# Kernel tuning notes

Hardware: AMD Instinct MI355X
Metric: run time of the kernel (lower is better)

## Reference

```python
import jax, jax.numpy as jnp
import numpy as np

D_MODEL, D_K, D_V, N_HEADS = 1024, 64, 64, 16
BATCH, N_CTX = 2, 2048


def half_causal_allowed(n):
    # rows [0, n/2): attend to cols [0, n/2) only (dense block)
    # rows [n/2, n): standard causal (col <= row)
    i = jnp.arange(n)[:, None]
    j = jnp.arange(n)[None, :]
    top = (i < n // 2) & (j < n // 2)
    bot = (i >= n // 2) & (j <= i)
    return top | bot  # [n, n] bool


def setup_inputs() -> dict:
    key = jax.random.key(0)
    ks = jax.random.split(key, 8)
    s_in = 1.0 / np.sqrt(D_MODEL)
    s_out = 1.0 / np.sqrt(D_V * N_HEADS)
    return {
        "x": jax.random.normal(ks[0], (BATCH, N_CTX, D_MODEL), jnp.float32),
        # Linear weights stored [in, out] (transpose of torch layout)
        "Wq": jax.random.uniform(ks[1], (D_MODEL, D_K * N_HEADS), jnp.float32, -s_in, s_in),
        "bq": jax.random.uniform(ks[2], (D_K * N_HEADS,), jnp.float32, -s_in, s_in),
        "Wk": jax.random.uniform(ks[3], (D_MODEL, D_K * N_HEADS), jnp.float32, -s_in, s_in),
        "bk": jax.random.uniform(ks[4], (D_K * N_HEADS,), jnp.float32, -s_in, s_in),
        "Wv": jax.random.uniform(ks[5], (D_MODEL, D_V * N_HEADS), jnp.float32, -s_in, s_in),
        "bv": jax.random.uniform(ks[6], (D_V * N_HEADS,), jnp.float32, -s_in, s_in),
        "Wo": jax.random.uniform(ks[7], (D_V * N_HEADS, D_MODEL), jnp.float32, -s_out, s_out),
    }


def reference(x, Wq, bq, Wk, bk, Wv, bv, Wo):
    b, n, _ = x.shape
    h, dk, dv = N_HEADS, D_K, D_V
    # projections -> [b, h, n, d]
    q = (x @ Wq + bq).reshape(b, n, h, dk).transpose(0, 2, 1, 3)
    k = (x @ Wk + bk).reshape(b, n, h, dk).transpose(0, 2, 1, 3)
    v = (x @ Wv + bv).reshape(b, n, h, dv).transpose(0, 2, 1, 3)
    scores = jnp.einsum("bhqd,bhkd->bhqk", q / jnp.sqrt(jnp.float32(dk)), k)
    allowed = half_causal_allowed(n)  # [n, n]
    scores = jnp.where(allowed, scores, -jnp.inf)
    attn = jax.nn.softmax(scores, axis=-1)  # dropout p=0 -> identity
    out = jnp.einsum("bhqk,bhkd->bhqd", attn, v)
    out = out.transpose(0, 2, 1, 3).reshape(b, n, h * dv)
    return out @ Wo  # final Linear has no bias
```

## Files before the change

### kernel.cpp

```cpp
#include <hip/hip_runtime.h>
#include <hip/hip_bf16.h>

#define NH 16
#define DH 64
#define DM 1024
#define NC 2048
#define MROWS 4096
#define KVT 64

#define SCALE_Q 0.180336880f

typedef __attribute__((ext_vector_type(8))) short short8;
typedef __attribute__((ext_vector_type(4))) float f32x4;
typedef __attribute__((ext_vector_type(16))) float f32x16;
typedef __attribute__((ext_vector_type(4))) unsigned int uint4e;

__device__ __forceinline__ unsigned pkbf16(float a, float b) {
    unsigned r;
    asm("v_cvt_pk_bf16_f32 %0, %1, %2" : "=v"(r) : "v"(a), "v"(b));
    return r;
}
__device__ __forceinline__ unsigned short f2bf(float x) {
    return (unsigned short)(pkbf16(x, x) & 0xffffu);
}
__device__ __forceinline__ float exp2v(float x) {
    float r;
    asm("v_exp_f32 %0, %1" : "=v"(r) : "v"(x));
    return r;
}
__device__ __forceinline__ f32x16 fzero16() {
    f32x16 r;
    #pragma unroll
    for (int i = 0; i < 16; ++i) r[i] = 0.f;
    return r;
}
__device__ __forceinline__ short8 mk8(unsigned w0, unsigned w1, unsigned w2, unsigned w3) {
    uint4e u = {w0, w1, w2, w3};
    return __builtin_bit_cast(short8, u);
}
__device__ __forceinline__ void gload16(const unsigned short* g, unsigned short* l) {
    __builtin_amdgcn_global_load_lds(
        (const __attribute__((address_space(1))) void*)g,
        (__attribute__((address_space(3))) void*)l, 16, 0, 0);
}

__global__ __launch_bounds__(256) void cvt_x(const float* __restrict__ in,
                                             unsigned short* __restrict__ out, int n8)
{
    int i = blockIdx.x * 256 + threadIdx.x;
    if (i >= n8) return;
    const float4 a = ((const float4*)in)[i * 2];
    const float4 b = ((const float4*)in)[i * 2 + 1];
    uint4e u = {pkbf16(a.x, a.y), pkbf16(a.z, a.w), pkbf16(b.x, b.y), pkbf16(b.z, b.w)};
    ((uint4e*)out)[i] = u;
}

__global__ __launch_bounds__(256) void cvt_w4(const float* __restrict__ W0,
                                              const float* __restrict__ W1,
                                              const float* __restrict__ W2,
                                              const float* __restrict__ W3,
                                              unsigned short* __restrict__ Wt4)
{
    __shared__ unsigned short T[64][72];
    const int z = blockIdx.z;
    const float* W = (z == 0) ? W0 : (z == 1) ? W1 : (z == 2) ? W2 : W3;
    unsigned short* Wt = Wt4 + (size_t)z * DM * DM;
    const int t = threadIdx.x;
    const int r = t >> 2, s = t & 3;
    const int bi = blockIdx.y;
    const int bj = blockIdx.x;
    const float* src = W + (size_t)(bi * 64 + r) * DM + bj * 64 + s * 16;
    float4 f0 = ((const float4*)src)[0];
    float4 f1 = ((const float4*)src)[1];
    float4 f2 = ((const float4*)src)[2];
    float4 f3 = ((const float4*)src)[3];
    uint2 u;
    u.x = pkbf16(f0.x, f0.y); u.y = pkbf16(f0.z, f0.w); *(uint2*)&T[r][s * 16]      = u;
    u.x = pkbf16(f1.x, f1.y); u.y = pkbf16(f1.z, f1.w); *(uint2*)&T[r][s * 16 + 4]  = u;
    u.x = pkbf16(f2.x, f2.y); u.y = pkbf16(f2.z, f2.w); *(uint2*)&T[r][s * 16 + 8]  = u;
    u.x = pkbf16(f3.x, f3.y); u.y = pkbf16(f3.z, f3.w); *(uint2*)&T[r][s * 16 + 12] = u;
    __syncthreads();
    unsigned short vals[16];
    #pragma unroll
    for (int j = 0; j < 16; ++j) vals[j] = T[s * 16 + j][r];
    unsigned short* dst = Wt + (size_t)(bj * 64 + r) * DM + bi * 64 + s * 16;
    *(short8*)(dst)     = *(short8*)&vals[0];
    *(short8*)(dst + 8) = *(short8*)&vals[8];
}

__global__ __launch_bounds__(256) void gemm_qkv(const unsigned short* __restrict__ A,
                                                const unsigned short* __restrict__ Bt,
                                                const float* __restrict__ bq,
                                                const float* __restrict__ bk,
                                                const float* __restrict__ bv,
                                                unsigned short* __restrict__ Out)
{
    __shared__ unsigned short As[128 * 32];
    __shared__ unsigned short Bs[128 * 32];
    const int t  = threadIdx.x;
    const int w  = t >> 6, l = t & 63;
    const int wr = w >> 1, wc = w & 1;
    const int m0 = blockIdx.y << 7;
    const int n0 = blockIdx.x << 7;

    f32x4 acc[4][4] = {};
    const int nkt = DM >> 5;
    for (int kt = 0; kt < nkt; ++kt) {
        #pragma unroll
        for (int j = 0; j < 2; ++j) {
            const int c0 = j * 256 + w * 64;
            const int cc = c0 + l;
            const int row = cc >> 2, qq = cc & 3;
            gload16(A  + (size_t)(m0 + row) * DM + kt * 32 + qq * 8, &As[c0 * 8]);
            gload16(Bt + (size_t)(n0 + row) * DM + kt * 32 + qq * 8, &Bs[c0 * 8]);
        }
        __syncthreads();
        short8 af[4], bf_[4];
        #pragma unroll
        for (int mi = 0; mi < 4; ++mi)
            af[mi] = *(short8*)&As[(wr * 64 + mi * 16 + (l & 15)) * 32 + (l >> 4) * 8];
        #pragma unroll
        for (int ni = 0; ni < 4; ++ni)
            bf_[ni] = *(short8*)&Bs[(wc * 64 + ni * 16 + (l & 15)) * 32 + (l >> 4) * 8];
        #pragma unroll
        for (int mi = 0; mi < 4; ++mi)
            #pragma unroll
            for (int ni = 0; ni < 4; ++ni)
                acc[mi][ni] = __builtin_amdgcn_mfma_f32_16x16x32_bf16(
                                  af[mi], bf_[ni], acc[mi][ni], 0, 0, 0);
        __syncthreads();
    }

    const int seg = n0 >> 10;
    const float* bias = (seg == 0) ? bq : (seg == 1) ? bk : bv;
    const float scale = (seg == 0) ? SCALE_Q : 1.0f;
    const int ncol0 = (n0 & 1023) + wc * 64;
    float bvv[4];
    #pragma unroll
    for (int ni = 0; ni < 4; ++ni)
        bvv[ni] = bias[ncol0 + ni * 16 + (l & 15)];

    if (seg == 2) {
        unsigned short* vt = Out + 2 * (size_t)MROWS * DM;
        #pragma unroll
        for (int mi = 0; mi < 4; ++mi)
            #pragma unroll
            for (int ni = 0; ni < 4; ++ni) {
                const int gcol = ncol0 + ni * 16 + (l & 15);
                const int h_ = gcol >> 6, d_ = gcol & 63;
                #pragma unroll
                for (int r = 0; r < 4; ++r) {
                    const int grow = m0 + wr * 64 + mi * 16 + (l >> 4) * 4 + r;
                    const int b_ = grow >> 11, n_ = grow & 2047;
                    vt[(((size_t)b_ * 16 + h_) * 64 + d_) * NC + n_] =
                        f2bf(acc[mi][ni][r] + bvv[ni]);
                }
            }
    } else {
        unsigned short* C = Out + (size_t)seg * MROWS * DM;
        #pragma unroll
        for (int mi = 0; mi < 4; ++mi)
            #pragma unroll
            for (int ni = 0; ni < 4; ++ni) {
                const int gcol = ncol0 + ni * 16 + (l & 15);
                #pragma unroll
                for (int r = 0; r < 4; ++r) {
                    const int grow = m0 + wr * 64 + mi * 16 + (l >> 4) * 4 + r;
                    C[(size_t)grow * DM + gcol] = f2bf((acc[mi][ni][r] + bvv[ni]) * scale);
                }
            }
    }
}

__global__ __launch_bounds__(256) void gemm_wo(const unsigned short* __restrict__ A,
                                               const unsigned short* __restrict__ Bt,
                                               float* __restrict__ C)
{
    __shared__ unsigned short As[64 * 32];
    __shared__ unsigned short Bs[128 * 32];
    const int t = threadIdx.x, w = t >> 6, l = t & 63;
    const int wr = w >> 1, wc = w & 1;
    const int m0 = blockIdx.y << 6;
    const int n0 = blockIdx.x << 7;

    f32x4 acc[2][4] = {};
    const int nkt = DM >> 5;
    for (int kt = 0; kt < nkt; ++kt) {
        {
            const int c0 = w * 64;
            const int cc = c0 + l;
            const int row = cc >> 2, qq = cc & 3;
            gload16(A + (size_t)(m0 + row) * DM + kt * 32 + qq * 8, &As[c0 * 8]);
        }
        #pragma unroll
        for (int j = 0; j < 2; ++j) {
            const int c0 = j * 256 + w * 64;
            const int cc = c0 + l;
            const int row = cc >> 2, qq = cc & 3;
            gload16(Bt + (size_t)(n0 + row) * DM + kt * 32 + qq * 8, &Bs[c0 * 8]);
        }
        __syncthreads();
        short8 af[2], bf_[4];
        #pragma unroll
        for (int mi = 0; mi < 2; ++mi)
            af[mi] = *(short8*)&As[(wr * 32 + mi * 16 + (l & 15)) * 32 + (l >> 4) * 8];
        #pragma unroll
        for (int ni = 0; ni < 4; ++ni)
            bf_[ni] = *(short8*)&Bs[(wc * 64 + ni * 16 + (l & 15)) * 32 + (l >> 4) * 8];
        #pragma unroll
        for (int mi = 0; mi < 2; ++mi)
            #pragma unroll
            for (int ni = 0; ni < 4; ++ni)
                acc[mi][ni] = __builtin_amdgcn_mfma_f32_16x16x32_bf16(
                                  af[mi], bf_[ni], acc[mi][ni], 0, 0, 0);
        __syncthreads();
    }
    #pragma unroll
    for (int mi = 0; mi < 2; ++mi)
        #pragma unroll
        for (int ni = 0; ni < 4; ++ni) {
            const int gcol = n0 + wc * 64 + ni * 16 + (l & 15);
            #pragma unroll
            for (int r = 0; r < 4; ++r) {
                const int grow = m0 + wr * 32 + mi * 16 + (l >> 4) * 4 + r;
                C[(size_t)grow * DM + gcol] = acc[mi][ni][r];
            }
        }
}

__global__ __launch_bounds__(128, 2) void attn_lds(const unsigned short* __restrict__ Qg,
                                                   const unsigned short* __restrict__ Kg,
                                                   const unsigned short* __restrict__ Vtg,
                                                   unsigned short* __restrict__ Og)
{
    __shared__ unsigned short KS[2][4096];
    __shared__ unsigned short VS[2][4096];
    const int t   = threadIdx.x;
    const int w   = t >> 6;
    const int l   = t & 63;
    const int l31 = l & 31;
    const int hi  = l >> 5;

    const int f   = blockIdx.x;
    const int xcd = f & 7;
    const int pos = f >> 3;
    const int bh  = xcd * 4 + (pos >> 5);
    int qt = pos & 31;
    if ((pos >> 5) & 1) qt = 31 - qt;
    const int b = bh >> 4;
    const int h = bh & 15;

    const int qb = qt << 6;
    const int wq = qb + w * 32;
    const size_t rb0 = (size_t)b * NC;
    const int hd = h * DH;

    const unsigned short* qp = Qg + (rb0 + wq + l31) * DM + hd + hi * 8;
    short8 fq[4];
    #pragma unroll
    for (int c = 0; c < 4; ++c)
        fq[c] = *(const short8*)(qp + c * 16);

    f32x16 o0 = fzero16(), o1 = fzero16();
    float mrun = -1e30f, lrun = 0.f;
    const bool bottom = (qb >= NC / 2);
    const int nkv = bottom ? (qt + 1) : 16;

    const unsigned short* Vbase = Vtg + (size_t)bh * 64 * NC;

    auto stage = [&](int it, int buf) {
        const int kb = it * KVT;
        #pragma unroll
        for (int j = 0; j < 4; ++j) {
            const int jj  = w * 4 + j;
            const int p   = jj * 64 + l;
            const int row = p >> 3;
            const int slot = (p & 7) ^ (row & 7);
            gload16(Kg + (size_t)(rb0 + kb + row) * DM + hd + slot * 8,
                    &KS[buf][jj * 512]);
            gload16(Vbase + (size_t)row * NC + kb + slot * 8,
                    &VS[buf][jj * 512]);
        }
    };

    stage(0, 0);
    __syncthreads();

    for (int it = 0; it < nkv; ++it) {
        const int kb = it * KVT;
        const int cur = it & 1;
        if (it + 1 < nkv) stage(it + 1, cur ^ 1);

        const unsigned short* Kb = &KS[cur][0];
        short8 kf[2][4];
        #pragma unroll
        for (int half = 0; half < 2; ++half) {
            const int row = half * 32 + l31;
            const int rx  = row & 7;
            #pragma unroll
            for (int c = 0; c < 4; ++c) {
                const int slot = (c * 2 + hi) ^ rx;
                kf[half][c] = *(const short8*)(Kb + row * 64 + slot * 8);
            }
        }
        f32x16 s0 = fzero16(), s1 = fzero16();
        __builtin_amdgcn_s_setprio(1);
        #pragma unroll
        for (int c = 0; c < 4; ++c) {
            s0 = __builtin_amdgcn_mfma_f32_32x32x16_bf16(kf[0][c], fq[c], s0, 0, 0, 0);
            s1 = __builtin_amdgcn_mfma_f32_32x32x16_bf16(kf[1][c], fq[c], s1, 0, 0, 0);
        }
        __builtin_amdgcn_s_setprio(0);
        if (bottom && (kb + KVT - 1 > wq)) {
            const int qg = wq + l31;
            #pragma unroll
            for (int r = 0; r < 16; ++r) {
                const int kk = (r & 3) + 8 * (r >> 2) + 4 * hi;
                if (kb + kk > qg)      s0[r] = -1e30f;
                if (kb + 32 + kk > qg) s1[r] = -1e30f;
            }
        }
        float tm[16];
        #pragma unroll
        for (int r = 0; r < 16; ++r) tm[r] = fmaxf(s0[r], s1[r]);
        #pragma unroll
        for (int st = 8; st > 0; st >>= 1)
            #pragma unroll
            for (int r = 0; r < 8; ++r)
                if (r < st) tm[r] = fmaxf(tm[r], tm[r + st]);
        float pm = fmaxf(tm[0], __shfl_xor(tm[0], 32));
        if (!__all(pm - mrun <= 8.f)) {
            const float mnew = fmaxf(mrun, pm);
            const float corr = exp2v(mrun - mnew);
            mrun = mnew;
            lrun *= corr;
            #pragma unroll
            for (int i = 0; i < 16; ++i) { o0[i] *= corr; o1[i] *= corr; }
        }
        float rs = 0.f;
        #pragma unroll
        for (int r = 0; r < 16; ++r) { s0[r] = exp2v(s0[r] - mrun); rs += s0[r]; }
        #pragma unroll
        for (int r = 0; r < 16; ++r) { s1[r] = exp2v(s1[r] - mrun); rs += s1[r]; }
        rs += __shfl_xor(rs, 32);
        lrun += rs;
        const unsigned short* Vb = &VS[cur][0];
        __builtin_amdgcn_s_setprio(1);
        #pragma unroll
        for (int kc = 0; kc < 4; ++kc) {
            const f32x16 src = (kc < 2) ? s0 : s1;
            const int rbase = (kc & 1) * 8;
            unsigned A01 = pkbf16(src[rbase + 0], src[rbase + 1]);
            unsigned A23 = pkbf16(src[rbase + 2], src[rbase + 3]);
            unsigned A45 = pkbf16(src[rbase + 4], src[rbase + 5]);
            unsigned A67 = pkbf16(src[rbase + 6], src[rbase + 7]);
            unsigned s01 = (unsigned)__shfl_xor((int)A01, 32);
            unsigned s23 = (unsigned)__shfl_xor((int)A23, 32);
            unsigned s45 = (unsigned)__shfl_xor((int)A45, 32);
            unsigned s67 = (unsigned)__shfl_xor((int)A67, 32);
            short8 fp = hi ? mk8(s45, s67, A45, A67)
                           : mk8(A01, A23, s01, s23);
            const int slot = (kc * 2 + hi);
            const int r0_ = l31, r1_ = 32 + l31;
            short8 v0 = *(const short8*)(Vb + r0_ * 64 + (slot ^ (r0_ & 7)) * 8);
            short8 v1 = *(const short8*)(Vb + r1_ * 64 + (slot ^ (r1_ & 7)) * 8);
            o0 = __builtin_amdgcn_mfma_f32_32x32x16_bf16(v0, fp, o0, 0, 0, 0);
            o1 = __builtin_amdgcn_mfma_f32_32x32x16_bf16(v1, fp, o1, 0, 0, 0);
        }
        __builtin_amdgcn_s_setprio(0);

        __syncthreads();
    }

    const float inv = 1.f / lrun;
    unsigned short* obuf = (unsigned short*)&KS[0][0];
    {
        unsigned short* reg = obuf + (size_t)(w * 32 + l31) * 72;
        #pragma unroll
        for (int r = 0; r < 16; ++r) {
            const int dd = (r & 3) + 8 * (r >> 2) + 4 * hi;
            reg[dd]      = f2bf(o0[r] * inv);
            reg[dd + 32] = f2bf(o1[r] * inv);
        }
    }
    __syncthreads();
    {
        const int row = t >> 1, seg = t & 1;
        const unsigned short* src = obuf + (size_t)row * 72 + seg * 32;
        unsigned short* dst = Og + (rb0 + qb + row) * DM + hd + seg * 32;
        #pragma unroll
        for (int i = 0; i < 4; ++i)
            *(short8*)(dst + i * 8) = *(const short8*)(src + i * 8);
    }
}

extern "C" void kernel_launch(void* const* d_in, const int* in_sizes, int n_in,
                              void* d_out, int out_size, void* d_ws, size_t ws_size,
                              hipStream_t stream)
{
    const float* x  = (const float*)d_in[0];
    const float* Wq = (const float*)d_in[1];
    const float* bq = (const float*)d_in[2];
    const float* Wk = (const float*)d_in[3];
    const float* bk = (const float*)d_in[4];
    const float* Wv = (const float*)d_in[5];
    const float* bv = (const float*)d_in[6];
    const float* Wo = (const float*)d_in[7];
    float* out = (float*)d_out;

    char* ws = (char*)d_ws;
    const size_t szA = (size_t)MROWS * DM * 2;
    const size_t szW = (size_t)DM * DM * 2;
    unsigned short* xb  = (unsigned short*)(ws);
    unsigned short* wqT = (unsigned short*)(ws + szA);
    unsigned short* woT = (unsigned short*)(ws + szA + 3 * szW);
    unsigned short* qb_ = (unsigned short*)(ws + szA + 4 * szW);
    unsigned short* kb_ = (unsigned short*)(ws + 2 * szA + 4 * szW);
    unsigned short* vt_ = (unsigned short*)(ws + 3 * szA + 4 * szW);
    unsigned short* ab_ = (unsigned short*)(ws + 4 * szA + 4 * szW);

    cvt_x<<<dim3(MROWS * DM / 8 / 256), 256, 0, stream>>>(x, xb, MROWS * DM / 8);
    cvt_w4<<<dim3(16, 16, 4), 256, 0, stream>>>(Wq, Wk, Wv, Wo, wqT);

    gemm_qkv<<<dim3(24, 32), 256, 0, stream>>>(xb, wqT, bq, bk, bv, qb_);
    attn_lds<<<dim3(1024), 128, 0, stream>>>(qb_, kb_, vt_, ab_);
    gemm_wo<<<dim3(8, 64), 256, 0, stream>>>(ab_, woT, out);
}
```

Before: 124.0 us.

## Convert attention to single-wave blocks with 32-row KV tiles and vmcnt waits

The attention kernel now uses 64-thread single-wave blocks, each owning 32 query rows, and launches twice as many blocks. KV tiles shrink to 32 keys, which halves LDS per block. Because only one wave runs per block, __syncthreads are dropped in favour of explicit s_waitcnt vmcnt waits on the double-buffered global-to-LDS loads. The aim is finer-grained load balance over the causal half and less barrier overhead, at the cost of more loop iterations, less K/V reuse across waves, and more global traffic for K/V.

```diff
diff --git a/kernel.cpp b/kernel.cpp
--- a/kernel.cpp
+++ b/kernel.cpp
@@ -6,7 +6,7 @@
 #define DM 1024
 #define NC 2048
 #define MROWS 4096
-#define KVT 64
+#define KVT 32
 
 #define SCALE_Q 0.180336880f
 
@@ -228,34 +228,31 @@
         }
 }
 
-__global__ __launch_bounds__(128, 2) void attn_lds(const unsigned short* __restrict__ Qg,
+__global__ __launch_bounds__(64, 2) void attn_wave(const unsigned short* __restrict__ Qg,
                                                    const unsigned short* __restrict__ Kg,
                                                    const unsigned short* __restrict__ Vtg,
                                                    unsigned short* __restrict__ Og)
 {
-    __shared__ unsigned short KS[2][4096];
-    __shared__ unsigned short VS[2][4096];
-    const int t   = threadIdx.x;
-    const int w   = t >> 6;
-    const int l   = t & 63;
+    __shared__ unsigned short KS[2][2048];
+    __shared__ unsigned short VS[2][2048];
+    const int l   = threadIdx.x;
     const int l31 = l & 31;
     const int hi  = l >> 5;
 
     const int f   = blockIdx.x;
     const int xcd = f & 7;
     const int pos = f >> 3;
-    const int bh  = xcd * 4 + (pos >> 5);
-    int qt = pos & 31;
-    if ((pos >> 5) & 1) qt = 31 - qt;
+    const int bh  = xcd * 4 + (pos >> 6);
+    int qt = pos & 63;
+    if ((pos >> 6) & 1) qt = 63 - qt;
     const int b = bh >> 4;
     const int h = bh & 15;
 
-    const int qb = qt << 6;
-    const int wq = qb + w * 32;
+    const int qb = qt << 5;
     const size_t rb0 = (size_t)b * NC;
     const int hd = h * DH;
 
-    const unsigned short* qp = Qg + (rb0 + wq + l31) * DM + hd + hi * 8;
+    const unsigned short* qp = Qg + (rb0 + qb + l31) * DM + hd + hi * 8;
     short8 fq[4];
     #pragma unroll
     for (int c = 0; c < 4; ++c)
@@ -264,7 +261,7 @@
     f32x16 o0 = fzero16(), o1 = fzero16();
     float mrun = -1e30f, lrun = 0.f;
     const bool bottom = (qb >= NC / 2);
-    const int nkv = bottom ? (qt + 1) : 16;
+    const int nkv = bottom ? (qt + 1) : 32;
 
     const unsigned short* Vbase = Vtg + (size_t)bh * 64 * NC;
 
@@ -272,61 +269,55 @@
         const int kb = it * KVT;
         #pragma unroll
         for (int j = 0; j < 4; ++j) {
-            const int jj  = w * 4 + j;
-            const int p   = jj * 64 + l;
-            const int row = p >> 3;
-            const int slot = (p & 7) ^ (row & 7);
-            gload16(Kg + (size_t)(rb0 + kb + row) * DM + hd + slot * 8,
-                    &KS[buf][jj * 512]);
-            gload16(Vbase + (size_t)row * NC + kb + slot * 8,
-                    &VS[buf][jj * 512]);
+            const int pk  = j * 64 + l;
+            const int krow = pk >> 3, kslot = (pk & 7) ^ (krow & 7);
+            gload16(Kg + (size_t)(rb0 + kb + krow) * DM + hd + kslot * 8,
+                    &KS[buf][j * 512]);
+            const int vrow = pk >> 2, vslot = (pk & 3) ^ (vrow & 3);
+            gload16(Vbase + (size_t)vrow * NC + kb + vslot * 8,
+                    &VS[buf][j * 512]);
         }
     };
 
     stage(0, 0);
-    __syncthreads();
 
     for (int it = 0; it < nkv; ++it) {
-        const int kb = it * KVT;
         const int cur = it & 1;
-        if (it + 1 < nkv) stage(it + 1, cur ^ 1);
+        if (it + 1 < nkv) {
+            stage(it + 1, cur ^ 1);
+            asm volatile("s_waitcnt vmcnt(8)" ::: "memory");
+        } else {
+            asm volatile("s_waitcnt vmcnt(0)" ::: "memory");
+        }
 
         const unsigned short* Kb = &KS[cur][0];
-        short8 kf[2][4];
-        #pragma unroll
-        for (int half = 0; half < 2; ++half) {
-            const int row = half * 32 + l31;
-            const int rx  = row & 7;
-            #pragma unroll
-            for (int c = 0; c < 4; ++c) {
-                const int slot = (c * 2 + hi) ^ rx;
-                kf[half][c] = *(const short8*)(Kb + row * 64 + slot * 8);
-            }
-        }
-        f32x16 s0 = fzero16(), s1 = fzero16();
+        const int rx = l31 & 7;
+        short8 kf[4];
+        #pragma unroll
+        for (int c = 0; c < 4; ++c) {
+            const int slot = (c * 2 + hi) ^ rx;
+            kf[c] = *(const short8*)(Kb + l31 * 64 + slot * 8);
+        }
+        f32x16 s0 = fzero16();
         __builtin_amdgcn_s_setprio(1);
         #pragma unroll
-        for (int c = 0; c < 4; ++c) {
-            s0 = __builtin_amdgcn_mfma_f32_32x32x16_bf16(kf[0][c], fq[c], s0, 0, 0, 0);
-            s1 = __builtin_amdgcn_mfma_f32_32x32x16_bf16(kf[1][c], fq[c], s1, 0, 0, 0);
-        }
+        for (int c = 0; c < 4; ++c)
+            s0 = __builtin_amdgcn_mfma_f32_32x32x16_bf16(kf[c], fq[c], s0, 0, 0, 0);
         __builtin_amdgcn_s_setprio(0);
-        if (bottom && (kb + KVT - 1 > wq)) {
-            const int qg = wq + l31;
+        if (bottom && it == qt) {
             #pragma unroll
             for (int r = 0; r < 16; ++r) {
                 const int kk = (r & 3) + 8 * (r >> 2) + 4 * hi;
-                if (kb + kk > qg)      s0[r] = -1e30f;
-                if (kb + 32 + kk > qg) s1[r] = -1e30f;
+                if (kk > l31) s0[r] = -1e30f;
             }
         }
-        float tm[16];
-        #pragma unroll
-        for (int r = 0; r < 16; ++r) tm[r] = fmaxf(s0[r], s1[r]);
-        #pragma unroll
-        for (int st = 8; st > 0; st >>= 1)
-            #pragma unroll
-            for (int r = 0; r < 8; ++r)
+        float tm[8];
+        #pragma unroll
+        for (int r = 0; r < 8; ++r) tm[r] = fmaxf(s0[r], s0[r + 8]);
+        #pragma unroll
+        for (int st = 4; st > 0; st >>= 1)
+            #pragma unroll
+            for (int r = 0; r < 4; ++r)
                 if (r < st) tm[r] = fmaxf(tm[r], tm[r + st]);
         float pm = fmaxf(tm[0], __shfl_xor(tm[0], 32));
         if (!__all(pm - mrun <= 8.f)) {
@@ -340,42 +331,35 @@
         float rs = 0.f;
         #pragma unroll
         for (int r = 0; r < 16; ++r) { s0[r] = exp2v(s0[r] - mrun); rs += s0[r]; }
-        #pragma unroll
-        for (int r = 0; r < 16; ++r) { s1[r] = exp2v(s1[r] - mrun); rs += s1[r]; }
         rs += __shfl_xor(rs, 32);
         lrun += rs;
         const unsigned short* Vb = &VS[cur][0];
+        unsigned pw[8], px[8];
+        #pragma unroll
+        for (int i = 0; i < 8; ++i)
+            pw[i] = pkbf16(s0[2 * i], s0[2 * i + 1]);
+        #pragma unroll
+        for (int i = 0; i < 8; ++i)
+            px[i] = (unsigned)__shfl_xor((int)pw[i], 32);
         __builtin_amdgcn_s_setprio(1);
         #pragma unroll
-        for (int kc = 0; kc < 4; ++kc) {
-            const f32x16 src = (kc < 2) ? s0 : s1;
-            const int rbase = (kc & 1) * 8;
-            unsigned A01 = pkbf16(src[rbase + 0], src[rbase + 1]);
-            unsigned A23 = pkbf16(src[rbase + 2], src[rbase + 3]);
-            unsigned A45 = pkbf16(src[rbase + 4], src[rbase + 5]);
-            unsigned A67 = pkbf16(src[rbase + 6], src[rbase + 7]);
-            unsigned s01 = (unsigned)__shfl_xor((int)A01, 32);
-            unsigned s23 = (unsigned)__shfl_xor((int)A23, 32);
-            unsigned s45 = (unsigned)__shfl_xor((int)A45, 32);
-            unsigned s67 = (unsigned)__shfl_xor((int)A67, 32);
-            short8 fp = hi ? mk8(s45, s67, A45, A67)
-                           : mk8(A01, A23, s01, s23);
-            const int slot = (kc * 2 + hi);
+        for (int j = 0; j < 2; ++j) {
+            short8 fp = hi ? mk8(px[j*4+2], px[j*4+3], pw[j*4+2], pw[j*4+3])
+                           : mk8(pw[j*4+0], pw[j*4+1], px[j*4+0], px[j*4+1]);
+            const int slot = j * 2 + hi;
             const int r0_ = l31, r1_ = 32 + l31;
-            short8 v0 = *(const short8*)(Vb + r0_ * 64 + (slot ^ (r0_ & 7)) * 8);
-            short8 v1 = *(const short8*)(Vb + r1_ * 64 + (slot ^ (r1_ & 7)) * 8);
+            short8 v0 = *(const short8*)(Vb + r0_ * 32 + ((slot ^ (r0_ & 3)) * 8));
+            short8 v1 = *(const short8*)(Vb + r1_ * 32 + ((slot ^ (r1_ & 3)) * 8));
             o0 = __builtin_amdgcn_mfma_f32_32x32x16_bf16(v0, fp, o0, 0, 0, 0);
             o1 = __builtin_amdgcn_mfma_f32_32x32x16_bf16(v1, fp, o1, 0, 0, 0);
         }
         __builtin_amdgcn_s_setprio(0);
-
-        __syncthreads();
     }
 
     const float inv = 1.f / lrun;
     unsigned short* obuf = (unsigned short*)&KS[0][0];
     {
-        unsigned short* reg = obuf + (size_t)(w * 32 + l31) * 72;
+        unsigned short* reg = obuf + (size_t)l31 * 72;
         #pragma unroll
         for (int r = 0; r < 16; ++r) {
             const int dd = (r & 3) + 8 * (r >> 2) + 4 * hi;
@@ -383,9 +367,8 @@
             reg[dd + 32] = f2bf(o1[r] * inv);
         }
     }
-    __syncthreads();
     {
-        const int row = t >> 1, seg = t & 1;
+        const int row = l >> 1, seg = l & 1;
         const unsigned short* src = obuf + (size_t)row * 72 + seg * 32;
         unsigned short* dst = Og + (rb0 + qb + row) * DM + hd + seg * 32;
         #pragma unroll
@@ -423,6 +406,6 @@
     cvt_w4<<<dim3(16, 16, 4), 256, 0, stream>>>(Wq, Wk, Wv, Wo, wqT);
 
     gemm_qkv<<<dim3(24, 32), 256, 0, stream>>>(xb, wqT, bq, bk, bv, qb_);
-    attn_lds<<<dim3(1024), 128, 0, stream>>>(qb_, kb_, vt_, ab_);
+    attn_wave<<<dim3(2048), 64, 0, stream>>>(qb_, kb_, vt_, ab_);
     gemm_wo<<<dim3(8, 64), 256, 0, stream>>>(ab_, woT, out);
 }
```

After: 138.4 us. 1.12x slower.

## Use single-wave attention blocks with register-staged K/V and no block barriers

Applied to the files above, without the earlier changes.

The attention kernel moves from two-wave 128-thread blocks with double-buffered LDS to single-wave 64-thread blocks, each handling 32 query rows, so twice as many blocks launch. K and V tiles are read from one LDS buffer into registers, and the next tile's global-to-LDS copy is issued right after those reads, which removes all __syncthreads. The causal mask is applied only on the last tile and the row-sum uses a tree reduction. In exchange, K/V global traffic per query row doubles, register pressure rises from holding V fragments, and overlap within one wave depends on explicit waitcnt ordering.

```diff
diff --git a/kernel.cpp b/kernel.cpp
--- a/kernel.cpp
+++ b/kernel.cpp
@@ -228,34 +228,31 @@
         }
 }
 
-__global__ __launch_bounds__(128, 2) void attn_lds(const unsigned short* __restrict__ Qg,
-                                                   const unsigned short* __restrict__ Kg,
-                                                   const unsigned short* __restrict__ Vtg,
-                                                   unsigned short* __restrict__ Og)
-{
-    __shared__ unsigned short KS[2][4096];
-    __shared__ unsigned short VS[2][4096];
-    const int t   = threadIdx.x;
-    const int w   = t >> 6;
-    const int l   = t & 63;
+__global__ __launch_bounds__(64, 2) void attn_sb(const unsigned short* __restrict__ Qg,
+                                                 const unsigned short* __restrict__ Kg,
+                                                 const unsigned short* __restrict__ Vtg,
+                                                 unsigned short* __restrict__ Og)
+{
+    __shared__ unsigned short KS[4096];
+    __shared__ unsigned short VS[4096];
+    const int l   = threadIdx.x;
     const int l31 = l & 31;
     const int hi  = l >> 5;
 
     const int f   = blockIdx.x;
     const int xcd = f & 7;
     const int pos = f >> 3;
-    const int bh  = xcd * 4 + (pos >> 5);
-    int qt = pos & 31;
-    if ((pos >> 5) & 1) qt = 31 - qt;
+    const int bh  = xcd * 4 + (pos >> 6);
+    int qt = pos & 63;
+    if ((pos >> 6) & 1) qt = 63 - qt;
     const int b = bh >> 4;
     const int h = bh & 15;
 
-    const int qb = qt << 6;
-    const int wq = qb + w * 32;
+    const int qb = qt << 5;
     const size_t rb0 = (size_t)b * NC;
     const int hd = h * DH;
 
-    const unsigned short* qp = Qg + (rb0 + wq + l31) * DM + hd + hi * 8;
+    const unsigned short* qp = Qg + (rb0 + qb + l31) * DM + hd + hi * 8;
     short8 fq[4];
     #pragma unroll
     for (int c = 0; c < 4; ++c)
@@ -264,35 +261,31 @@
     f32x16 o0 = fzero16(), o1 = fzero16();
     float mrun = -1e30f, lrun = 0.f;
     const bool bottom = (qb >= NC / 2);
-    const int nkv = bottom ? (qt + 1) : 16;
+    const int nkv = bottom ? ((qt >> 1) + 1) : 16;
 
     const unsigned short* Vbase = Vtg + (size_t)bh * 64 * NC;
 
-    auto stage = [&](int it, int buf) {
+    auto stage = [&](int it) {
         const int kb = it * KVT;
         #pragma unroll
-        for (int j = 0; j < 4; ++j) {
-            const int jj  = w * 4 + j;
-            const int p   = jj * 64 + l;
-            const int row = p >> 3;
+        for (int j = 0; j < 8; ++j) {
+            const int p    = j * 64 + l;
+            const int row  = p >> 3;
             const int slot = (p & 7) ^ (row & 7);
             gload16(Kg + (size_t)(rb0 + kb + row) * DM + hd + slot * 8,
-                    &KS[buf][jj * 512]);
+                    &KS[j * 512]);
             gload16(Vbase + (size_t)row * NC + kb + slot * 8,
-                    &VS[buf][jj * 512]);
+                    &VS[j * 512]);
         }
     };
 
-    stage(0, 0);
-    __syncthreads();
+    stage(0);
 
     for (int it = 0; it < nkv; ++it) {
         const int kb = it * KVT;
-        const int cur = it & 1;
-        if (it + 1 < nkv) stage(it + 1, cur ^ 1);
-
-        const unsigned short* Kb = &KS[cur][0];
-        short8 kf[2][4];
+        asm volatile("s_waitcnt vmcnt(0)" ::: "memory");
+
+        short8 kf[2][4], vf[2][4];
         #pragma unroll
         for (int half = 0; half < 2; ++half) {
             const int row = half * 32 + l31;
@@ -300,9 +293,14 @@
             #pragma unroll
             for (int c = 0; c < 4; ++c) {
                 const int slot = (c * 2 + hi) ^ rx;
-                kf[half][c] = *(const short8*)(Kb + row * 64 + slot * 8);
+                kf[half][c] = *(const short8*)(&KS[row * 64 + slot * 8]);
+                vf[half][c] = *(const short8*)(&VS[row * 64 + slot * 8]);
             }
         }
+        asm volatile("s_waitcnt lgkmcnt(0)" ::: "memory");
+        __builtin_amdgcn_sched_barrier(0);
+        if (it + 1 < nkv) stage(it + 1);
+
         f32x16 s0 = fzero16(), s1 = fzero16();
         __builtin_amdgcn_s_setprio(1);
         #pragma unroll
@@ -311,8 +309,9 @@
             s1 = __builtin_amdgcn_mfma_f32_32x32x16_bf16(kf[1][c], fq[c], s1, 0, 0, 0);
         }
         __builtin_amdgcn_s_setprio(0);
-        if (bottom && (kb + KVT - 1 > wq)) {
-            const int qg = wq + l31;
+
+        if (bottom && it == nkv - 1) {
+            const int qg = qb + l31;
             #pragma unroll
             for (int r = 0; r < 16; ++r) {
                 const int kk = (r & 3) + 8 * (r >> 2) + 4 * hi;
@@ -337,14 +336,20 @@
             #pragma unroll
             for (int i = 0; i < 16; ++i) { o0[i] *= corr; o1[i] *= corr; }
         }
-        float rs = 0.f;
-        #pragma unroll
-        for (int r = 0; r < 16; ++r) { s0[r] = exp2v(s0[r] - mrun); rs += s0[r]; }
-        #pragma unroll
-        for (int r = 0; r < 16; ++r) { s1[r] = exp2v(s1[r] - mrun); rs += s1[r]; }
-        rs += __shfl_xor(rs, 32);
-        lrun += rs;
-        const unsigned short* Vb = &VS[cur][0];
+        #pragma unroll
+        for (int r = 0; r < 16; ++r) s0[r] = exp2v(s0[r] - mrun);
+        #pragma unroll
+        for (int r = 0; r < 16; ++r) s1[r] = exp2v(s1[r] - mrun);
+        float t16[16];
+        #pragma unroll
+        for (int r = 0; r < 16; ++r) t16[r] = s0[r] + s1[r];
+        #pragma unroll
+        for (int st = 8; st > 0; st >>= 1)
+            #pragma unroll
+            for (int r = 0; r < 8; ++r)
+                if (r < st) t16[r] += t16[r + st];
+        lrun += t16[0] + __shfl_xor(t16[0], 32);
+
         __builtin_amdgcn_s_setprio(1);
         #pragma unroll
         for (int kc = 0; kc < 4; ++kc) {
@@ -360,22 +365,16 @@
             unsigned s67 = (unsigned)__shfl_xor((int)A67, 32);
             short8 fp = hi ? mk8(s45, s67, A45, A67)
                            : mk8(A01, A23, s01, s23);
-            const int slot = (kc * 2 + hi);
-            const int r0_ = l31, r1_ = 32 + l31;
-            short8 v0 = *(const short8*)(Vb + r0_ * 64 + (slot ^ (r0_ & 7)) * 8);
-            short8 v1 = *(const short8*)(Vb + r1_ * 64 + (slot ^ (r1_ & 7)) * 8);
-            o0 = __builtin_amdgcn_mfma_f32_32x32x16_bf16(v0, fp, o0, 0, 0, 0);
-            o1 = __builtin_amdgcn_mfma_f32_32x32x16_bf16(v1, fp, o1, 0, 0, 0);
+            o0 = __builtin_amdgcn_mfma_f32_32x32x16_bf16(vf[0][kc], fp, o0, 0, 0, 0);
+            o1 = __builtin_amdgcn_mfma_f32_32x32x16_bf16(vf[1][kc], fp, o1, 0, 0, 0);
         }
         __builtin_amdgcn_s_setprio(0);
-
-        __syncthreads();
     }
 
     const float inv = 1.f / lrun;
-    unsigned short* obuf = (unsigned short*)&KS[0][0];
+    unsigned short* obuf = &KS[0];
     {
-        unsigned short* reg = obuf + (size_t)(w * 32 + l31) * 72;
+        unsigned short* reg = obuf + (size_t)l31 * 72;
         #pragma unroll
         for (int r = 0; r < 16; ++r) {
             const int dd = (r & 3) + 8 * (r >> 2) + 4 * hi;
@@ -383,9 +382,8 @@
             reg[dd + 32] = f2bf(o1[r] * inv);
         }
     }
-    __syncthreads();
     {
-        const int row = t >> 1, seg = t & 1;
+        const int row = l >> 1, seg = l & 1;
         const unsigned short* src = obuf + (size_t)row * 72 + seg * 32;
         unsigned short* dst = Og + (rb0 + qb + row) * DM + hd + seg * 32;
         #pragma unroll
@@ -423,6 +421,6 @@
     cvt_w4<<<dim3(16, 16, 4), 256, 0, stream>>>(Wq, Wk, Wv, Wo, wqT);
 
     gemm_qkv<<<dim3(24, 32), 256, 0, stream>>>(xb, wqT, bq, bk, bv, qb_);
-    attn_lds<<<dim3(1024), 128, 0, stream>>>(qb_, kb_, vt_, ab_);
+    attn_sb<<<dim3(2048), 64, 0, stream>>>(qb_, kb_, vt_, ab_);
     gemm_wo<<<dim3(8, 64), 256, 0, stream>>>(ab_, woT, out);
 }
```

Result: no change. 126.0 us (+1.6%).

## Deepen attention KV prefetch to two tiles with explicit waitcnt barriers

Applied to the files above, without the earlier changes.

The attention kernel now prefetches two KV tiles ahead. It waits on the vector-memory counter with an explicit vmcnt and raw s_barrier instead of __syncthreads. K and V fragments are read into registers up front, so the LDS buffer can be refilled with tile it+2 right after a second barrier while the MFMAs run. Per-wave tiles that lie entirely above the causal diagonal are skipped, and the row-sum reduction is restructured into a tree. The risks are higher register pressure from holding V fragments and correctness that depends on the hand-set vmcnt(8) matching the number of async loads issued per stage.

```diff
diff --git a/kernel.cpp b/kernel.cpp
--- a/kernel.cpp
+++ b/kernel.cpp
@@ -228,10 +228,10 @@
         }
 }
 
-__global__ __launch_bounds__(128, 2) void attn_lds(const unsigned short* __restrict__ Qg,
-                                                   const unsigned short* __restrict__ Kg,
-                                                   const unsigned short* __restrict__ Vtg,
-                                                   unsigned short* __restrict__ Og)
+__global__ __launch_bounds__(128, 2) void attn_pipe(const unsigned short* __restrict__ Qg,
+                                                    const unsigned short* __restrict__ Kg,
+                                                    const unsigned short* __restrict__ Vtg,
+                                                    unsigned short* __restrict__ Og)
 {
     __shared__ unsigned short KS[2][4096];
     __shared__ unsigned short VS[2][4096];
@@ -284,15 +284,19 @@
     };
 
     stage(0, 0);
-    __syncthreads();
+    if (nkv > 1) stage(1, 1);
 
     for (int it = 0; it < nkv; ++it) {
         const int kb = it * KVT;
         const int cur = it & 1;
-        if (it + 1 < nkv) stage(it + 1, cur ^ 1);
-
-        const unsigned short* Kb = &KS[cur][0];
-        short8 kf[2][4];
+        if (it + 1 < nkv) {
+            asm volatile("s_waitcnt vmcnt(8)" ::: "memory");
+        } else {
+            asm volatile("s_waitcnt vmcnt(0)" ::: "memory");
+        }
+        __builtin_amdgcn_s_barrier();
+
+        short8 kf[2][4], vf[2][4];
         #pragma unroll
         for (int half = 0; half < 2; ++half) {
             const int row = half * 32 + l31;
@@ -300,77 +304,87 @@
             #pragma unroll
             for (int c = 0; c < 4; ++c) {
                 const int slot = (c * 2 + hi) ^ rx;
-                kf[half][c] = *(const short8*)(Kb + row * 64 + slot * 8);
-            }
-        }
-        f32x16 s0 = fzero16(), s1 = fzero16();
-        __builtin_amdgcn_s_setprio(1);
-        #pragma unroll
-        for (int c = 0; c < 4; ++c) {
-            s0 = __builtin_amdgcn_mfma_f32_32x32x16_bf16(kf[0][c], fq[c], s0, 0, 0, 0);
-            s1 = __builtin_amdgcn_mfma_f32_32x32x16_bf16(kf[1][c], fq[c], s1, 0, 0, 0);
-        }
-        __builtin_amdgcn_s_setprio(0);
-        if (bottom && (kb + KVT - 1 > wq)) {
-            const int qg = wq + l31;
-            #pragma unroll
-            for (int r = 0; r < 16; ++r) {
-                const int kk = (r & 3) + 8 * (r >> 2) + 4 * hi;
-                if (kb + kk > qg)      s0[r] = -1e30f;
-                if (kb + 32 + kk > qg) s1[r] = -1e30f;
-            }
-        }
-        float tm[16];
-        #pragma unroll
-        for (int r = 0; r < 16; ++r) tm[r] = fmaxf(s0[r], s1[r]);
-        #pragma unroll
-        for (int st = 8; st > 0; st >>= 1)
-            #pragma unroll
-            for (int r = 0; r < 8; ++r)
-                if (r < st) tm[r] = fmaxf(tm[r], tm[r + st]);
-        float pm = fmaxf(tm[0], __shfl_xor(tm[0], 32));
-        if (!__all(pm - mrun <= 8.f)) {
-            const float mnew = fmaxf(mrun, pm);
-            const float corr = exp2v(mrun - mnew);
-            mrun = mnew;
-            lrun *= corr;
-            #pragma unroll
-            for (int i = 0; i < 16; ++i) { o0[i] *= corr; o1[i] *= corr; }
-        }
-        float rs = 0.f;
-        #pragma unroll
-        for (int r = 0; r < 16; ++r) { s0[r] = exp2v(s0[r] - mrun); rs += s0[r]; }
-        #pragma unroll
-        for (int r = 0; r < 16; ++r) { s1[r] = exp2v(s1[r] - mrun); rs += s1[r]; }
-        rs += __shfl_xor(rs, 32);
-        lrun += rs;
-        const unsigned short* Vb = &VS[cur][0];
-        __builtin_amdgcn_s_setprio(1);
-        #pragma unroll
-        for (int kc = 0; kc < 4; ++kc) {
-            const f32x16 src = (kc < 2) ? s0 : s1;
-            const int rbase = (kc & 1) * 8;
-            unsigned A01 = pkbf16(src[rbase + 0], src[rbase + 1]);
-            unsigned A23 = pkbf16(src[rbase + 2], src[rbase + 3]);
-            unsigned A45 = pkbf16(src[rbase + 4], src[rbase + 5]);
-            unsigned A67 = pkbf16(src[rbase + 6], src[rbase + 7]);
-            unsigned s01 = (unsigned)__shfl_xor((int)A01, 32);
-            unsigned s23 = (unsigned)__shfl_xor((int)A23, 32);
-            unsigned s45 = (unsigned)__shfl_xor((int)A45, 32);
-            unsigned s67 = (unsigned)__shfl_xor((int)A67, 32);
-            short8 fp = hi ? mk8(s45, s67, A45, A67)
-                           : mk8(A01, A23, s01, s23);
-            const int slot = (kc * 2 + hi);
-            const int r0_ = l31, r1_ = 32 + l31;
-            short8 v0 = *(const short8*)(Vb + r0_ * 64 + (slot ^ (r0_ & 7)) * 8);
-            short8 v1 = *(const short8*)(Vb + r1_ * 64 + (slot ^ (r1_ & 7)) * 8);
-            o0 = __builtin_amdgcn_mfma_f32_32x32x16_bf16(v0, fp, o0, 0, 0, 0);
-            o1 = __builtin_amdgcn_mfma_f32_32x32x16_bf16(v1, fp, o1, 0, 0, 0);
-        }
-        __builtin_amdgcn_s_setprio(0);
-
-        __syncthreads();
-    }
+                kf[half][c] = *(const short8*)(&KS[cur][row * 64 + slot * 8]);
+                vf[half][c] = *(const short8*)(&VS[cur][row * 64 + slot * 8]);
+            }
+        }
+        asm volatile("s_waitcnt lgkmcnt(0)" ::: "memory");
+        __builtin_amdgcn_sched_barrier(0);
+        __builtin_amdgcn_s_barrier();
+
+        if (it + 2 < nkv) stage(it + 2, cur);
+
+        const bool active = bottom ? (kb <= wq + 31) : true;
+        if (active) {
+            f32x16 s0 = fzero16(), s1 = fzero16();
+            __builtin_amdgcn_s_setprio(1);
+            #pragma unroll
+            for (int c = 0; c < 4; ++c) {
+                s0 = __builtin_amdgcn_mfma_f32_32x32x16_bf16(kf[0][c], fq[c], s0, 0, 0, 0);
+                s1 = __builtin_amdgcn_mfma_f32_32x32x16_bf16(kf[1][c], fq[c], s1, 0, 0, 0);
+            }
+            __builtin_amdgcn_s_setprio(0);
+            if (bottom && (kb + KVT - 1 > wq)) {
+                const int qg = wq + l31;
+                #pragma unroll
+                for (int r = 0; r < 16; ++r) {
+                    const int kk = (r & 3) + 8 * (r >> 2) + 4 * hi;
+                    if (kb + kk > qg)      s0[r] = -1e30f;
+                    if (kb + 32 + kk > qg) s1[r] = -1e30f;
+                }
+            }
+            float tm[16];
+            #pragma unroll
+            for (int r = 0; r < 16; ++r) tm[r] = fmaxf(s0[r], s1[r]);
+            #pragma unroll
+            for (int st = 8; st > 0; st >>= 1)
+                #pragma unroll
+                for (int r = 0; r < 8; ++r)
+                    if (r < st) tm[r] = fmaxf(tm[r], tm[r + st]);
+            float pm = fmaxf(tm[0], __shfl_xor(tm[0], 32));
+            if (!__all(pm - mrun <= 8.f)) {
+                const float mnew = fmaxf(mrun, pm);
+                const float corr = exp2v(mrun - mnew);
+                mrun = mnew;
+                lrun *= corr;
+                #pragma unroll
+                for (int i = 0; i < 16; ++i) { o0[i] *= corr; o1[i] *= corr; }
+            }
+            #pragma unroll
+            for (int r = 0; r < 16; ++r) s0[r] = exp2v(s0[r] - mrun);
+            #pragma unroll
+            for (int r = 0; r < 16; ++r) s1[r] = exp2v(s1[r] - mrun);
+            float t16[16];
+            #pragma unroll
+            for (int r = 0; r < 16; ++r) t16[r] = s0[r] + s1[r];
+            #pragma unroll
+            for (int st = 8; st > 0; st >>= 1)
+                #pragma unroll
+                for (int r = 0; r < 8; ++r)
+                    if (r < st) t16[r] += t16[r + st];
+            lrun += t16[0] + __shfl_xor(t16[0], 32);
+            __builtin_amdgcn_s_setprio(1);
+            #pragma unroll
+            for (int kc = 0; kc < 4; ++kc) {
+                const f32x16 src = (kc < 2) ? s0 : s1;
+                const int rbase = (kc & 1) * 8;
+                unsigned A01 = pkbf16(src[rbase + 0], src[rbase + 1]);
+                unsigned A23 = pkbf16(src[rbase + 2], src[rbase + 3]);
+                unsigned A45 = pkbf16(src[rbase + 4], src[rbase + 5]);
+                unsigned A67 = pkbf16(src[rbase + 6], src[rbase + 7]);
+                unsigned s01 = (unsigned)__shfl_xor((int)A01, 32);
+                unsigned s23 = (unsigned)__shfl_xor((int)A23, 32);
+                unsigned s45 = (unsigned)__shfl_xor((int)A45, 32);
+                unsigned s67 = (unsigned)__shfl_xor((int)A67, 32);
+                short8 fp = hi ? mk8(s45, s67, A45, A67)
+                               : mk8(A01, A23, s01, s23);
+                o0 = __builtin_amdgcn_mfma_f32_32x32x16_bf16(vf[0][kc], fp, o0, 0, 0, 0);
+                o1 = __builtin_amdgcn_mfma_f32_32x32x16_bf16(vf[1][kc], fp, o1, 0, 0, 0);
+            }
+            __builtin_amdgcn_s_setprio(0);
+        }
+    }
+    __syncthreads();
 
     const float inv = 1.f / lrun;
     unsigned short* obuf = (unsigned short*)&KS[0][0];
@@ -423,6 +437,6 @@
     cvt_w4<<<dim3(16, 16, 4), 256, 0, stream>>>(Wq, Wk, Wv, Wo, wqT);
 
     gemm_qkv<<<dim3(24, 32), 256, 0, stream>>>(xb, wqT, bq, bk, bv, qb_);
-    attn_lds<<<dim3(1024), 128, 0, stream>>>(qb_, kb_, vt_, ab_);
+    attn_pipe<<<dim3(1024), 128, 0, stream>>>(qb_, kb_, vt_, ab_);
     gemm_wo<<<dim3(8, 64), 256, 0, stream>>>(ab_, woT, out);
 }
```

Measured after the change: 122.7 us. About the same (-1.1%).
